# Kernel optimization log

Hardware: AMD Instinct MI355X
Metric: run time of the kernel (lower is better)

Reference implementation:

```python
import jax, jax.numpy as jnp
import numpy as np

N_HEAD = 12

def setup_inputs() -> dict:
    key = jax.random.key(0)
    k1, k2, k3 = jax.random.split(key, 3)
    B, T, C = 8, 1024, 768
    x = jax.random.normal(k1, (B, T, C), dtype=jnp.float32)
    W_attn = jax.random.normal(k2, (3 * C, C), dtype=jnp.float32) * 0.02
    b_attn = jax.random.normal(k3, (3 * C,), dtype=jnp.float32) * 0.02
    return {"x": x, "W_attn": W_attn, "b_attn": b_attn}

def reference(x, W_attn, b_attn):
    B, T, C = x.shape
    hd = C // N_HEAD
    # qkv projection: Linear(C, 3C)
    qkv = x @ W_attn.T + b_attn  # (B, T, 3C)
    q, k, v = jnp.split(qkv, 3, axis=-1)
    def to_heads(t):
        return t.reshape(B, T, N_HEAD, hd).transpose(0, 2, 1, 3)  # (B, H, T, hd)
    q, k, v = to_heads(q), to_heads(k), to_heads(v)
    scale = 1.0 / jnp.sqrt(jnp.asarray(hd, dtype=x.dtype))
    att = jnp.einsum('bhqd,bhkd->bhqk', q * scale, k)  # (B, H, T, T)
    causal = jnp.tril(jnp.ones((T, T), dtype=bool))
    # causal mask then ReLU (no softmax)
    att = jnp.where(causal, jnp.maximum(att, 0.0), 0.0)
    y = jnp.einsum('bhqk,bhkd->bhqd', att, v)  # (B, H, T, hd)
    return y.transpose(0, 2, 1, 3).reshape(B, T, C)
```

## Files before the change

kernel.cpp:

```cpp
#include <hip/hip_runtime.h>
#include <hip/hip_bf16.h>
#include <stdint.h>

typedef __attribute__((ext_vector_type(8))) short short8;
typedef __attribute__((ext_vector_type(4))) float f32x4;

#define N_HEADS 12
#define HD      64
#define BSZ     8
#define TSZ     1024
#define CSZ     768
#define MSZ     (BSZ * TSZ)
#define N3      (3 * CSZ)

static __device__ __forceinline__ unsigned short f2bf(float f) {
    union { float f; uint32_t u; } v; v.f = f;
    uint32_t r = v.u + 0x7fffu + ((v.u >> 16) & 1u);
    return (unsigned short)(r >> 16);
}

static __device__ __forceinline__ void gload16(const unsigned short* g,
                                               unsigned short* l) {
    __builtin_amdgcn_global_load_lds(
        (const __attribute__((address_space(1))) void*)g,
        (__attribute__((address_space(3))) void*)l, 16, 0, 0);
}

__global__ void cvt2_f32_to_bf16(const float* __restrict__ x, int nx,
                                 const float* __restrict__ W, int nw,
                                 unsigned short* __restrict__ xb,
                                 unsigned short* __restrict__ wb) {
    int i = (blockIdx.x * blockDim.x + threadIdx.x) * 8;
    const float* s; unsigned short* d; int j;
    if (i < nx) { s = x; d = xb; j = i; }
    else        { s = W; d = wb; j = i - nx; if (j + 7 >= nw) return; }
    float4 f0 = *reinterpret_cast<const float4*>(s + j);
    float4 f1 = *reinterpret_cast<const float4*>(s + j + 4);
    ushort4 u0, u1;
    u0.x = f2bf(f0.x); u0.y = f2bf(f0.y); u0.z = f2bf(f0.z); u0.w = f2bf(f0.w);
    u1.x = f2bf(f1.x); u1.y = f2bf(f1.y); u1.z = f2bf(f1.z); u1.w = f2bf(f1.w);
    *reinterpret_cast<ushort4*>(d + j) = u0;
    *reinterpret_cast<ushort4*>(d + j + 4) = u1;
}

__global__ __launch_bounds__(512, 2) void qkv_gemm(
    const unsigned short* __restrict__ xb,
    const unsigned short* __restrict__ wb,
    const float* __restrict__ bias,
    unsigned short* __restrict__ qo,
    unsigned short* __restrict__ ko,
    unsigned short* __restrict__ vto)
{
    __shared__ unsigned short A0[128 * 64];
    __shared__ unsigned short B0[128 * 64];
    __shared__ unsigned short A1[128 * 64];
    __shared__ unsigned short B1[128 * 64];
    const int tid = threadIdx.x;
    const int lane = tid & 63;
    const int w = tid >> 6;
    const int lr = lane >> 4, lc = lane & 15;
    const int xcd = blockIdx.x & 7, idx = blockIdx.x >> 3;
    const int bm = xcd * 8 + (idx & 7);
    const int bn = idx >> 3;
    const int m0 = bm * 128;
    const int n0 = bn * 128;
    const int wrow = (w >> 2) * 64;
    const int wcol = (w & 3) * 32;

    const int r1 = tid >> 3, c1 = ((tid & 7) ^ (r1 & 7)) * 8;
    const int r2 = 64 + r1,  c2 = ((tid & 7) ^ (r2 & 7)) * 8;

    f32x4 acc[4][2] = {};

#define STAGE(T, LA, LB)                                                   \
    do {                                                                   \
        gload16(xb + (size_t)(m0 + r1) * CSZ + (T) * 64 + c1, (LA) + tid * 8); \
        gload16(xb + (size_t)(m0 + r2) * CSZ + (T) * 64 + c2, (LA) + 4096 + tid * 8); \
        gload16(wb + (size_t)(n0 + r1) * CSZ + (T) * 64 + c1, (LB) + tid * 8); \
        gload16(wb + (size_t)(n0 + r2) * CSZ + (T) * 64 + c2, (LB) + 4096 + tid * 8); \
    } while (0)

#define PHASE(T, CA, CB, DO_STAGE, VMN)                                    \
    do {                                                                   \
        short8 af[4][2], bf[2][2];                                         \
        _Pragma("unroll")                                                  \
        for (int mi = 0; mi < 4; ++mi)                                     \
            _Pragma("unroll")                                              \
            for (int ks = 0; ks < 2; ++ks) {                               \
                int row = wrow + mi * 16 + lc;                             \
                af[mi][ks] = *reinterpret_cast<const short8*>(             \
                    (CA) + row * 64 + (((ks * 4 + lr) ^ (row & 7)) * 8));  \
            }                                                              \
        _Pragma("unroll")                                                  \
        for (int ni = 0; ni < 2; ++ni)                                     \
            _Pragma("unroll")                                              \
            for (int ks = 0; ks < 2; ++ks) {                               \
                int row = wcol + ni * 16 + lc;                             \
                bf[ni][ks] = *reinterpret_cast<const short8*>(             \
                    (CB) + row * 64 + (((ks * 4 + lr) ^ (row & 7)) * 8));  \
            }                                                              \
        asm volatile("s_waitcnt lgkmcnt(0)" ::: "memory");                 \
        __builtin_amdgcn_sched_barrier(0);                                 \
        __builtin_amdgcn_s_barrier();          \
        if (DO_STAGE) STAGE((T) + 2, CA, CB);                              \
        __builtin_amdgcn_s_setprio(1);                                     \
        _Pragma("unroll")                                                  \
        for (int ks = 0; ks < 2; ++ks)                                     \
            _Pragma("unroll")                                              \
            for (int mi = 0; mi < 4; ++mi)                                 \
                _Pragma("unroll")                                          \
                for (int ni = 0; ni < 2; ++ni)                             \
                    acc[mi][ni] = __builtin_amdgcn_mfma_f32_16x16x32_bf16( \
                        af[mi][ks], bf[ni][ks], acc[mi][ni], 0, 0, 0);     \
        __builtin_amdgcn_s_setprio(0);                                     \
        asm volatile("s_waitcnt vmcnt(" #VMN ")" ::: "memory");            \
        __builtin_amdgcn_s_barrier();               \
        __builtin_amdgcn_sched_barrier(0);                                 \
    } while (0)

    STAGE(0, A0, B0);
    STAGE(1, A1, B1);
    asm volatile("s_waitcnt vmcnt(4)" ::: "memory");
    __builtin_amdgcn_s_barrier();

    #pragma unroll 1
    for (int tt = 0; tt < 10; tt += 2) {
        PHASE(tt,     A0, B0, true, 4);
        PHASE(tt + 1, A1, B1, true, 4);
    }
    PHASE(10, A0, B0, false, 0);
    PHASE(11, A1, B1, false, 0);
#undef STAGE
#undef PHASE

    const int sec = n0 / CSZ;
    const int nb = n0 - sec * CSZ;
    #pragma unroll
    for (int ni = 0; ni < 2; ++ni) {
        int ncol = wcol + ni * 16 + lc;
        int nn = nb + ncol;
        float badd = bias[n0 + ncol];
        int h = nn >> 6, d = nn & 63;
        #pragma unroll
        for (int mi = 0; mi < 4; ++mi) {
            int mbase = m0 + wrow + mi * 16 + lr * 4;
            int bb = mbase >> 10, t0 = mbase & 1023;
            int plane = bb * N_HEADS + h;
            if (sec == 0) {
                #pragma unroll
                for (int r = 0; r < 4; ++r)
                    qo[((size_t)plane * TSZ + t0 + r) * HD + d] =
                        f2bf((acc[mi][ni][r] + badd) * 0.125f);
            } else if (sec == 1) {
                #pragma unroll
                for (int r = 0; r < 4; ++r)
                    ko[((size_t)plane * TSZ + t0 + r) * HD + d] =
                        f2bf(acc[mi][ni][r] + badd);
            } else {
                ushort4 pk;
                pk.x = f2bf(acc[mi][ni][0] + badd);
                pk.y = f2bf(acc[mi][ni][1] + badd);
                pk.z = f2bf(acc[mi][ni][2] + badd);
                pk.w = f2bf(acc[mi][ni][3] + badd);
                *reinterpret_cast<ushort4*>(
                    vto + ((size_t)plane * HD + d) * TSZ + t0) = pk;
            }
        }
    }
}

__global__ __launch_bounds__(256, 3) void attn_kernel(
    const unsigned short* __restrict__ q,
    const unsigned short* __restrict__ k,
    const unsigned short* __restrict__ vt,
    float* __restrict__ out)
{
    __shared__ unsigned short Kl[2][64 * 64];
    __shared__ unsigned short Vl[2][64 * 64];
    __shared__ unsigned short Sl[4][32 * 64];
    const int tid = threadIdx.x;
    const int wid = tid >> 6;
    const int lane = tid & 63;
    const int lr = lane >> 4, lc = lane & 15;
    const int xcd = blockIdx.x & 7, slot = blockIdx.x >> 3;
    const int bh = xcd * 12 + (slot >> 3);
    const int s_ = slot & 7, rnd = slot >> 5;
    int pr;
    if (rnd == 0)      pr = s_;
    else if (rnd == 1) pr = (s_ + 3) & 7;
    else               pr = (5440239u >> (3 * s_)) & 7;
    const int jj = pr * 2 + (wid >> 1);
    const int b = bh / N_HEADS, h = bh - b * N_HEADS;
    const size_t base = (size_t)bh * (TSZ * HD);
    const size_t vbase = (size_t)bh * (HD * TSZ);
    const int qrow0 = jj * 64 + (wid & 1) * 32;
    unsigned short* sm = Sl[wid];
    const int ntb = pr * 2 + 2;
    const int ntw = jj + 1;

    short8 aq[2][2];
    #pragma unroll
    for (int ks = 0; ks < 2; ++ks)
        #pragma unroll
        for (int qi = 0; qi < 2; ++qi)
            aq[ks][qi] = *reinterpret_cast<const short8*>(
                q + base + (size_t)(qrow0 + qi * 16 + lc) * HD + ks * 32 + lr * 8);

    f32x4 y[2][4] = {};

#define STAGEKV(KT, BI)                                                     \
    do {                                                                    \
        _Pragma("unroll")                                                   \
        for (int i = 0; i < 2; ++i) {                                       \
            int c = i * 256 + tid;                                          \
            int r_ = c >> 3;                                                \
            int c8 = (c & 7) ^ (r_ & 7);                                    \
            gload16(k + base + (size_t)((KT) * 64 + r_) * HD + c8 * 8,      \
                    Kl[BI] + c * 8);                                        \
            gload16(vt + vbase + (size_t)r_ * TSZ + (KT) * 64 + c8 * 8,     \
                    Vl[BI] + c * 8);                                        \
        }                                                                   \
    } while (0)

    STAGEKV(0, 0);
    __syncthreads();

    for (int kt = 0; kt < ntb; ++kt) {
        const int bi = kt & 1;
        if (kt + 1 < ntb) STAGEKV(kt + 1, bi ^ 1);
        if (kt < ntw) {
            const unsigned short* Kb = Kl[bi];
            const unsigned short* Vb = Vl[bi];
            f32x4 st[4][2] = {};
            #pragma unroll
            for (int ks = 0; ks < 2; ++ks) {
                short8 ak[4];
                #pragma unroll
                for (int ki = 0; ki < 4; ++ki)
                    ak[ki] = *reinterpret_cast<const short8*>(
                        Kb + (ki * 16 + lc) * 64 + (((ks * 4 + lr) ^ (lc & 7)) * 8));
                __builtin_amdgcn_s_setprio(1);
                #pragma unroll
                for (int ki = 0; ki < 4; ++ki)
                    #pragma unroll
                    for (int qi = 0; qi < 2; ++qi)
                        st[ki][qi] = __builtin_amdgcn_mfma_f32_16x16x32_bf16(
                            ak[ki], aq[ks][qi], st[ki][qi], 0, 0, 0);
                __builtin_amdgcn_s_setprio(0);
            }
            const bool diag = (kt == jj);
            const int kv0 = kt * 64;
            #pragma unroll
            for (int ki = 0; ki < 4; ++ki) {
                #pragma unroll
                for (int qi = 0; qi < 2; ++qi) {
                    float vv[4];
                    #pragma unroll
                    for (int r = 0; r < 4; ++r) {
                        float s = fmaxf(st[ki][qi][r], 0.0f);
                        if (diag && (kv0 + ki * 16 + lr * 4 + r > qrow0 + qi * 16 + lc))
                            s = 0.0f;
                        vv[r] = s;
                    }
                    __hip_bfloat162 p0 = __float22bfloat162_rn(make_float2(vv[0], vv[1]));
                    __hip_bfloat162 p1 = __float22bfloat162_rn(make_float2(vv[2], vv[3]));
                    uint2 pk;
                    pk.x = *reinterpret_cast<unsigned*>(&p0);
                    pk.y = *reinterpret_cast<unsigned*>(&p1);
                    int row = qi * 16 + lc;
                    int chunk = (2 * ki + (lr >> 1)) ^ (row & 7);
                    *reinterpret_cast<uint2*>(
                        sm + row * 64 + chunk * 8 + (lr & 1) * 4) = pk;
                }
            }
            #pragma unroll
            for (int ks = 0; ks < 2; ++ks) {
                short8 as[2], bv[4];
                #pragma unroll
                for (int qi = 0; qi < 2; ++qi)
                    as[qi] = *reinterpret_cast<const short8*>(
                        sm + (qi * 16 + lc) * 64 + (((ks * 4 + lr) ^ (lc & 7)) * 8));
                #pragma unroll
                for (int di = 0; di < 4; ++di)
                    bv[di] = *reinterpret_cast<const short8*>(
                        Vb + (di * 16 + lc) * 64 + (((ks * 4 + lr) ^ (lc & 7)) * 8));
                __builtin_amdgcn_s_setprio(1);
                #pragma unroll
                for (int qi = 0; qi < 2; ++qi)
                    #pragma unroll
                    for (int di = 0; di < 4; ++di)
                        y[qi][di] = __builtin_amdgcn_mfma_f32_16x16x32_bf16(
                            as[qi], bv[di], y[qi][di], 0, 0, 0);
                __builtin_amdgcn_s_setprio(0);
            }
        }
        __syncthreads();
    }
#undef STAGEKV

    #pragma unroll
    for (int qi = 0; qi < 2; ++qi)
        #pragma unroll
        for (int di = 0; di < 4; ++di)
            #pragma unroll
            for (int r = 0; r < 4; ++r) {
                int t = qrow0 + qi * 16 + lr * 4 + r;
                int d = di * 16 + lc;
                out[((size_t)b * TSZ + t) * CSZ + h * HD + d] = y[qi][di][r];
            }
}

extern "C" void kernel_launch(void* const* d_in, const int* in_sizes, int n_in,
                              void* d_out, int out_size, void* d_ws, size_t ws_size,
                              hipStream_t stream) {
    const float* x    = (const float*)d_in[0];
    const float* W    = (const float*)d_in[1];
    const float* bias = (const float*)d_in[2];
    float* out = (float*)d_out;

    unsigned short* xb  = (unsigned short*)d_ws;
    unsigned short* wb  = xb + (size_t)MSZ * CSZ;
    unsigned short* qo  = wb + (size_t)N3 * CSZ;
    unsigned short* ko  = qo + (size_t)MSZ * CSZ;
    unsigned short* vto = ko + (size_t)MSZ * CSZ;

    const int nx = MSZ * CSZ;
    const int nw = N3 * CSZ;
    cvt2_f32_to_bf16<<<(nx + nw) / 2048, 256, 0, stream>>>(x, nx, W, nw, xb, wb);
    qkv_gemm<<<dim3(1152), 512, 0, stream>>>(xb, wb, bias, qo, ko, vto);
    attn_kernel<<<dim3(768), 256, 0, stream>>>(qo, ko, vto, out);
}
```

Baseline: 78.85 us.

## Load weight fragments straight from global memory and raise occupancy bound

The QKV GEMM no longer stages the weight (B) tile through shared memory. Each lane now reads its B fragments straight from global memory into registers at the start of every phase, which halves the LDS footprint and the per-stage async copies. The launch bound is also raised from 2 to 6 blocks per CU so more workgroups can be resident. The trade-off is that the global loads sit just before the MFMAs with no prefetch, so their latency is exposed. Weight data is also fetched redundantly by the waves that share a column slice, and the tighter register budget may cause spills.

New measurement: 187.0 us. +137.2%, slower.

```diff
diff --git a/kernel.cpp b/kernel.cpp
--- a/kernel.cpp
+++ b/kernel.cpp
@@ -43,7 +43,7 @@
     *reinterpret_cast<ushort4*>(d + j + 4) = u1;
 }
 
-__global__ __launch_bounds__(512, 2) void qkv_gemm(
+__global__ __launch_bounds__(512, 6) void qkv_gemm(
     const unsigned short* __restrict__ xb,
     const unsigned short* __restrict__ wb,
     const float* __restrict__ bias,
@@ -52,9 +52,7 @@
     unsigned short* __restrict__ vto)
 {
     __shared__ unsigned short A0[128 * 64];
-    __shared__ unsigned short B0[128 * 64];
     __shared__ unsigned short A1[128 * 64];
-    __shared__ unsigned short B1[128 * 64];
     const int tid = threadIdx.x;
     const int lane = tid & 63;
     const int w = tid >> 6;
@@ -70,19 +68,26 @@
     const int r1 = tid >> 3, c1 = ((tid & 7) ^ (r1 & 7)) * 8;
     const int r2 = 64 + r1,  c2 = ((tid & 7) ^ (r2 & 7)) * 8;
 
+    const unsigned short* wbase = wb + (size_t)(n0 + wcol + lc) * CSZ + lr * 8;
+
     f32x4 acc[4][2] = {};
 
-#define STAGE(T, LA, LB)                                                   \
+#define STAGE(T, LA)                                                       \
     do {                                                                   \
         gload16(xb + (size_t)(m0 + r1) * CSZ + (T) * 64 + c1, (LA) + tid * 8); \
         gload16(xb + (size_t)(m0 + r2) * CSZ + (T) * 64 + c2, (LA) + 4096 + tid * 8); \
-        gload16(wb + (size_t)(n0 + r1) * CSZ + (T) * 64 + c1, (LB) + tid * 8); \
-        gload16(wb + (size_t)(n0 + r2) * CSZ + (T) * 64 + c2, (LB) + 4096 + tid * 8); \
     } while (0)
 
-#define PHASE(T, CA, CB, DO_STAGE, VMN)                                    \
+#define PHASE(T, CA, DO_STAGE, VMN)                                        \
     do {                                                                   \
-        short8 af[4][2], bf[2][2];                                         \
+        short8 bf[2][2];                                                   \
+        _Pragma("unroll")                                                  \
+        for (int ni = 0; ni < 2; ++ni)                                     \
+            _Pragma("unroll")                                              \
+            for (int ks = 0; ks < 2; ++ks)                                 \
+                bf[ni][ks] = *reinterpret_cast<const short8*>(             \
+                    wbase + (size_t)(ni * 16) * CSZ + (T) * 64 + ks * 32); \
+        short8 af[4][2];                                                   \
         _Pragma("unroll")                                                  \
         for (int mi = 0; mi < 4; ++mi)                                     \
             _Pragma("unroll")                                              \
@@ -91,18 +96,10 @@
                 af[mi][ks] = *reinterpret_cast<const short8*>(             \
                     (CA) + row * 64 + (((ks * 4 + lr) ^ (row & 7)) * 8));  \
             }                                                              \
-        _Pragma("unroll")                                                  \
-        for (int ni = 0; ni < 2; ++ni)                                     \
-            _Pragma("unroll")                                              \
-            for (int ks = 0; ks < 2; ++ks) {                               \
-                int row = wcol + ni * 16 + lc;                             \
-                bf[ni][ks] = *reinterpret_cast<const short8*>(             \
-                    (CB) + row * 64 + (((ks * 4 + lr) ^ (row & 7)) * 8));  \
-            }                                                              \
         asm volatile("s_waitcnt lgkmcnt(0)" ::: "memory");                 \
         __builtin_amdgcn_sched_barrier(0);                                 \
-        __builtin_amdgcn_s_barrier();          \
-        if (DO_STAGE) STAGE((T) + 2, CA, CB);                              \
+        __builtin_amdgcn_s_barrier();        \
+        if (DO_STAGE) STAGE((T) + 2, CA);                                  \
         __builtin_amdgcn_s_setprio(1);                                     \
         _Pragma("unroll")                                                  \
         for (int ks = 0; ks < 2; ++ks)                                     \
@@ -114,22 +111,22 @@
                         af[mi][ks], bf[ni][ks], acc[mi][ni], 0, 0, 0);     \
         __builtin_amdgcn_s_setprio(0);                                     \
         asm volatile("s_waitcnt vmcnt(" #VMN ")" ::: "memory");            \
-        __builtin_amdgcn_s_barrier();               \
+        __builtin_amdgcn_s_barrier();             \
         __builtin_amdgcn_sched_barrier(0);                                 \
     } while (0)
 
-    STAGE(0, A0, B0);
-    STAGE(1, A1, B1);
-    asm volatile("s_waitcnt vmcnt(4)" ::: "memory");
+    STAGE(0, A0);
+    STAGE(1, A1);
+    asm volatile("s_waitcnt vmcnt(2)" ::: "memory");
     __builtin_amdgcn_s_barrier();
 
     #pragma unroll 1
     for (int tt = 0; tt < 10; tt += 2) {
-        PHASE(tt,     A0, B0, true, 4);
-        PHASE(tt + 1, A1, B1, true, 4);
+        PHASE(tt,     A0, true, 2);
+        PHASE(tt + 1, A1, true, 2);
     }
-    PHASE(10, A0, B0, false, 0);
-    PHASE(11, A1, B1, false, 0);
+    PHASE(10, A0, false, 0);
+    PHASE(11, A1, false, 0);
 #undef STAGE
 #undef PHASE
 
```
